# Optimization experiments

Hardware: AMD Instinct MI355X
Metric: run time of the kernel (lower is better)

The kernel has to match this reference:

```python
import jax, jax.numpy as jnp
import numpy as np

D = 512
H = 4 * D
EPS = 1e-5

def layernorm(x, g, b):
    mu = jnp.mean(x, axis=-1, keepdims=True)
    var = jnp.mean((x - mu) ** 2, axis=-1, keepdims=True)
    return (x - mu) * jax.lax.rsqrt(var + EPS) * g + b

def setup_inputs() -> dict:
    key = jax.random.key(0)
    ks = jax.random.split(key, 16)
    s = 0.02
    inp = {
        "x": jax.random.normal(ks[0], (16, 2048, D), dtype=jnp.float32),
        "wq": jax.random.normal(ks[1], (D, D), dtype=jnp.float32) * s,
        "bq": jnp.zeros((D,), jnp.float32),
        "wk": jax.random.normal(ks[2], (D, D), dtype=jnp.float32) * s,
        "bk": jnp.zeros((D,), jnp.float32),
        "wv": jax.random.normal(ks[3], (D, D), dtype=jnp.float32) * s,
        "bv": jnp.zeros((D,), jnp.float32),
        "wp": jax.random.normal(ks[4], (D, D), dtype=jnp.float32) * s,
        "bp": jnp.zeros((D,), jnp.float32),
        "w1": jax.random.normal(ks[5], (D, H), dtype=jnp.float32) * s,
        "b1": jnp.zeros((H,), jnp.float32),
        "w2": jax.random.normal(ks[6], (H, D), dtype=jnp.float32) * s,
        "b2": jnp.zeros((D,), jnp.float32),
        "g1": jnp.ones((D,), jnp.float32),
        "be1": jnp.zeros((D,), jnp.float32),
        "g2": jnp.ones((D,), jnp.float32),
        "be2": jnp.zeros((D,), jnp.float32),
    }
    return inp

def reference(x, wq, bq, wk, bk, wv, bv, wp, bp, w1, b1, w2, b2, g1, be1, g2, be2):
    temperature = jnp.sqrt(jnp.asarray(D, x.dtype))
    q = x @ wq + bq                      # [B,N,D]
    k = x @ wk + bk
    v = x @ wv + bv
    energy = jnp.einsum('bnd,bmd->bnm', q / temperature, k)   # [B,N,N]
    attn = jax.nn.softmax(energy, axis=-1)
    out = jnp.einsum('bnm,bmd->bnd', attn, v)
    att = out @ wp + bp
    x = layernorm(x + att, g1, be1)
    h = jax.nn.gelu(x @ w1 + b1, approximate=False)
    ff = h @ w2 + b2
    x = layernorm(x + ff, g2, be2)
    return x
```

## Files before the change

### kernel.cpp

```cpp
#include <hip/hip_runtime.h>
#include <cmath>

typedef __bf16 bf16_t;
typedef __bf16 bf16x8 __attribute__((ext_vector_type(8)));
typedef __bf16 bf16x4 __attribute__((ext_vector_type(4)));
typedef float f32x4 __attribute__((ext_vector_type(4)));

#define DEV_INLINE __device__ __forceinline__

DEV_INLINE void gload_lds16(const void* g, void* l) {
  __builtin_amdgcn_global_load_lds(
      (const __attribute__((address_space(1))) void*)g,
      (__attribute__((address_space(3))) void*)l, 16, 0, 0);
}

DEV_INLINE float gelu_f(float v) {
  const float u = v * (0.7978845608f + 0.0356774081f * v * v);
  const float e = __expf(2.f * u);
  const float th = 1.f - 2.f / (e + 1.f);
  return 0.5f * v * (1.f + th);
}

template<int EPI, bool HAS_BIAS>
__global__ __launch_bounds__(256, 2)
void gemm_bt(const bf16_t* __restrict__ A, const bf16_t* __restrict__ B,
             const float* __restrict__ bias, void* __restrict__ C,
             bf16_t* __restrict__ vTaux,
             int M, int N, int K, int lda, int ldb, int ldc,
             long sA, long sB, long sC, float scale)
{
  constexpr bool SWAP = (EPI == 1 || EPI == 2 || EPI == 3);
  __shared__ alignas(16) bf16_t lds[3][2][4096];
  const int b = blockIdx.z;
  A += (long)b * sA;
  B += (long)b * sB;
  const int t  = threadIdx.x;
  const int l  = t & 63;
  const int w  = t >> 6;
  const int wr = (w >> 1) * 64;
  const int wc = (w & 1) * 64;

  const int gx  = gridDim.x;
  const int nwg = gx * gridDim.y;
  int id = blockIdx.y * gx + blockIdx.x;
  id = (id & 7) * (nwg >> 3) + (id >> 3);
  const int m0 = (id / gx) * 128;
  const int n0 = (id % gx) * 128;

  const int r0 = t >> 2;
  const int r1 = r0 + 64;
  const int wb = (t & 3) * 16;
  const int cbs0 = wb ^ (((r0 >> 1) & 3) << 4);
  const int cbs1 = wb ^ (((r1 >> 1) & 3) << 4);
  const bf16_t* gA0 = A + (long)(m0 + r0) * lda + (cbs0 >> 1);
  const bf16_t* gA1 = A + (long)(m0 + r1) * lda + (cbs1 >> 1);
  const bf16_t* gB0 = B + (long)(n0 + r0) * ldb + (cbs0 >> 1);
  const bf16_t* gB1 = B + (long)(n0 + r1) * ldb + (cbs1 >> 1);

#define STAGE(kt, q) do {                                   \
    const long kofs_ = (long)(kt) * 32;                     \
    gload_lds16(gA0 + kofs_, &lds[q][0][t * 8]);            \
    gload_lds16(gA1 + kofs_, &lds[q][0][2048 + t * 8]);     \
    gload_lds16(gB0 + kofs_, &lds[q][1][t * 8]);            \
    gload_lds16(gB1 + kofs_, &lds[q][1][2048 + t * 8]);     \
  } while (0)

  const int fr  = l & 15;
  const int kkb = (l >> 4) * 16;
  int offA[4], offB[4];
#pragma unroll
  for (int mi = 0; mi < 4; mi++) {
    const int row = wr + mi * 16 + fr;
    offA[mi] = row * 32 + ((kkb ^ (((row >> 1) & 3) << 4)) >> 1);
  }
#pragma unroll
  for (int ni = 0; ni < 4; ni++) {
    const int row = wc + ni * 16 + fr;
    offB[ni] = row * 32 + ((kkb ^ (((row >> 1) & 3) << 4)) >> 1);
  }

  f32x4 acc[4][4] = {};

  const int NT = K >> 5;
  STAGE(0, 0);
  STAGE(1, 1);

  int q = 0;
  for (int kt = 0; kt < NT; ++kt) {
    if (kt < NT - 1) asm volatile("s_waitcnt vmcnt(4)" ::: "memory");
    else             asm volatile("s_waitcnt vmcnt(0)" ::: "memory");
    __builtin_amdgcn_sched_barrier(0);
    __builtin_amdgcn_s_barrier();

    if (kt + 2 < NT) {
      int qs = q + 2; if (qs >= 3) qs -= 3;
      STAGE(kt + 2, qs);
    }

    bf16x8 af[4], bfr[4];
#pragma unroll
    for (int mi = 0; mi < 4; mi++)
      af[mi] = *(const bf16x8*)&lds[q][0][offA[mi]];
#pragma unroll
    for (int ni = 0; ni < 4; ni++)
      bfr[ni] = *(const bf16x8*)&lds[q][1][offB[ni]];
#pragma unroll
    for (int mi = 0; mi < 4; mi++)
#pragma unroll
      for (int ni = 0; ni < 4; ni++) {
        if constexpr (SWAP)
          acc[mi][ni] = __builtin_amdgcn_mfma_f32_16x16x32_bf16(
              bfr[ni], af[mi], acc[mi][ni], 0, 0, 0);
        else
          acc[mi][ni] = __builtin_amdgcn_mfma_f32_16x16x32_bf16(
              af[mi], bfr[ni], acc[mi][ni], 0, 0, 0);
      }

    if (++q == 3) q = 0;
  }
#undef STAGE

  const long cb = (long)b * sC;

  if constexpr (SWAP) {
    const int cq = (l >> 4) * 4;
#pragma unroll
    for (int mi = 0; mi < 4; mi++) {
      const int row = m0 + wr + mi * 16 + fr;
      bf16_t* crow = (bf16_t*)C + cb + (long)row * ldc;
#pragma unroll
      for (int ni = 0; ni < 4; ni++) {
        const int c0 = n0 + wc + ni * 16 + cq;
        float4 b4 = {0.f, 0.f, 0.f, 0.f};
        if constexpr (HAS_BIAS) b4 = *(const float4*)&bias[c0];
        float vv[4] = { acc[mi][ni][0] + b4.x, acc[mi][ni][1] + b4.y,
                        acc[mi][ni][2] + b4.z, acc[mi][ni][3] + b4.w };
        if constexpr (EPI == 2) {
#pragma unroll
          for (int r = 0; r < 4; r++) vv[r] *= scale;
        }
        if constexpr (EPI == 3) {
#pragma unroll
          for (int r = 0; r < 4; r++) vv[r] = gelu_f(vv[r]);
        }
        bf16x4 pk = { (bf16_t)vv[0], (bf16_t)vv[1],
                      (bf16_t)vv[2], (bf16_t)vv[3] };
        *(bf16x4*)(crow + c0) = pk;
      }
    }
    return;
  }

  const int rbase = m0 + wr + (l >> 4) * 4;
#pragma unroll
  for (int mi = 0; mi < 4; mi++) {
    const int row0 = rbase + mi * 16;
#pragma unroll
    for (int ni = 0; ni < 4; ni++) {
      const int c = n0 + wc + ni * 16 + fr;
      float bias_v = 0.f;
      if constexpr (HAS_BIAS) bias_v = bias[c];
      float vals[4];
#pragma unroll
      for (int r = 0; r < 4; r++) vals[r] = acc[mi][ni][r] + bias_v;
      if (c < 1024) {
#pragma unroll
        for (int r = 0; r < 4; r++)
          ((bf16_t*)C)[(long)(row0 + r) * ldc + c] = (bf16_t)vals[r];
      } else {
        const int bb = row0 >> 11;
        const int n  = row0 & 2047;
        bf16x4 pk = { (bf16_t)vals[0], (bf16_t)vals[1],
                      (bf16_t)vals[2], (bf16_t)vals[3] };
        *(bf16x4*)&vTaux[(long)bb * (512 * 2048) + (long)(c - 1024) * 2048 + n] = pk;
      }
    }
  }
}

__global__ __launch_bounds__(256)
void transpose_cast(const float* __restrict__ in, bf16_t* __restrict__ out,
                    int R, int Cc)
{
  __shared__ float tile[32][33];
  const int c0 = blockIdx.x * 32;
  const int r0 = blockIdx.y * 32;
  const int tx = threadIdx.x & 31;
  const int ty = threadIdx.x >> 5;
#pragma unroll
  for (int i = 0; i < 32; i += 8)
    tile[ty + i][tx] = in[(long)(r0 + ty + i) * Cc + (c0 + tx)];
  __syncthreads();
#pragma unroll
  for (int i = 0; i < 32; i += 8)
    out[(long)(c0 + ty + i) * R + (r0 + tx)] = (bf16_t)tile[tx][ty + i];
}

__global__ __launch_bounds__(256)
void cast_to_bf16(const float* __restrict__ in, bf16_t* __restrict__ out, long n)
{
  const long i = ((long)blockIdx.x * 256 + threadIdx.x) * 4;
  if (i >= n) return;
  const float4 v = *(const float4*)&in[i];
  bf16x4 o = { (bf16_t)v.x, (bf16_t)v.y, (bf16_t)v.z, (bf16_t)v.w };
  *(bf16x4*)&out[i] = o;
}

__global__ __launch_bounds__(256)
void concat_bias(const float* __restrict__ a, const float* __restrict__ b,
                 const float* __restrict__ c, float* __restrict__ o)
{
  const int i = blockIdx.x * 256 + threadIdx.x;
  if (i < 512) o[i] = a[i];
  else if (i < 1024) o[i] = b[i - 512];
  else if (i < 1536) o[i] = c[i - 1024];
}

__global__ __launch_bounds__(256)
void softmax2048(bf16_t* __restrict__ E)
{
  const long row = blockIdx.x;
  bf16_t* p = E + row * 2048;
  const int t = threadIdx.x;
  bf16x8 xv = *(const bf16x8*)&p[t * 8];
  float v[8];
#pragma unroll
  for (int j = 0; j < 8; j++) v[j] = (float)xv[j];
  float m = v[0];
#pragma unroll
  for (int j = 1; j < 8; j++) m = fmaxf(m, v[j]);
  for (int o = 32; o; o >>= 1) m = fmaxf(m, __shfl_xor(m, o));
  __shared__ float redm[4];
  __shared__ float reds[4];
  if ((t & 63) == 0) redm[t >> 6] = m;
  __syncthreads();
  m = fmaxf(fmaxf(redm[0], redm[1]), fmaxf(redm[2], redm[3]));
  float s = 0.f;
#pragma unroll
  for (int j = 0; j < 8; j++) { v[j] = __expf(v[j] - m); s += v[j]; }
  for (int o = 32; o; o >>= 1) s += __shfl_xor(s, o);
  if ((t & 63) == 0) reds[t >> 6] = s;
  __syncthreads();
  s = reds[0] + reds[1] + reds[2] + reds[3];
  const float inv = 1.f / s;
  bf16x8 ov;
#pragma unroll
  for (int j = 0; j < 8; j++) ov[j] = (bf16_t)(v[j] * inv);
  *(bf16x8*)&p[t * 8] = ov;
}

template<bool EMIT_F32, bool EMIT_BF16>
__global__ __launch_bounds__(128)
void add_ln(const bf16_t* __restrict__ xa, const bf16_t* __restrict__ xadd,
            const float* __restrict__ g, const float* __restrict__ be,
            float* __restrict__ y, bf16_t* __restrict__ yb)
{
  const long row = blockIdx.x;
  const int c = threadIdx.x * 4;
  bf16x4 a = *(const bf16x4*)&xa[row * 512 + c];
  bf16x4 d = *(const bf16x4*)&xadd[row * 512 + c];
  float vv[4];
#pragma unroll
  for (int j = 0; j < 4; j++) vv[j] = (float)a[j] + (float)d[j];
  float s = 0.f, s2 = 0.f;
#pragma unroll
  for (int j = 0; j < 4; j++) { s += vv[j]; s2 += vv[j] * vv[j]; }
  for (int o = 32; o; o >>= 1) { s += __shfl_xor(s, o); s2 += __shfl_xor(s2, o); }
  __shared__ float r0[2], r1[2];
  const int w = threadIdx.x >> 6;
  if ((threadIdx.x & 63) == 0) { r0[w] = s; r1[w] = s2; }
  __syncthreads();
  s = r0[0] + r0[1]; s2 = r1[0] + r1[1];
  const float mu = s * (1.f / 512.f);
  const float var = s2 * (1.f / 512.f) - mu * mu;
  const float rstd = rsqrtf(var + 1e-5f);
  const float4 gg = *(const float4*)&g[c];
  const float4 bev = *(const float4*)&be[c];
  float o0 = (vv[0] - mu) * rstd * gg.x + bev.x;
  float o1 = (vv[1] - mu) * rstd * gg.y + bev.y;
  float o2 = (vv[2] - mu) * rstd * gg.z + bev.z;
  float o3 = (vv[3] - mu) * rstd * gg.w + bev.w;
  if constexpr (EMIT_F32) {
    float4 yo = { o0, o1, o2, o3 };
    *(float4*)&y[row * 512 + c] = yo;
  }
  if constexpr (EMIT_BF16) {
    bf16x4 ob = { (bf16_t)o0, (bf16_t)o1, (bf16_t)o2, (bf16_t)o3 };
    *(bf16x4*)&yb[row * 512 + c] = ob;
  }
}

extern "C" void kernel_launch(void* const* d_in, const int* in_sizes, int n_in,
                              void* d_out, int out_size, void* d_ws, size_t ws_size,
                              hipStream_t stream)
{
  const float* x   = (const float*)d_in[0];
  const float* wq  = (const float*)d_in[1];
  const float* bq  = (const float*)d_in[2];
  const float* wk  = (const float*)d_in[3];
  const float* bk  = (const float*)d_in[4];
  const float* wv  = (const float*)d_in[5];
  const float* bv  = (const float*)d_in[6];
  const float* wp  = (const float*)d_in[7];
  const float* bp  = (const float*)d_in[8];
  const float* w1  = (const float*)d_in[9];
  const float* b1  = (const float*)d_in[10];
  const float* w2  = (const float*)d_in[11];
  const float* b2  = (const float*)d_in[12];
  const float* g1  = (const float*)d_in[13];
  const float* be1 = (const float*)d_in[14];
  const float* g2  = (const float*)d_in[15];
  const float* be2 = (const float*)d_in[16];

  const long S = 16L * 2048 * 512;
  const long Mi = 1L << 20;

  const size_t NEED = (size_t)232 * Mi;
  if (ws_size < NEED) return;

  char* wsp = (char*)d_ws;
  bf16_t* wqkvT = (bf16_t*)(wsp + 0);
  bf16_t* wpT   = wqkvT + 1536L * 512;
  bf16_t* w1T   = wpT + 512L * 512;
  bf16_t* w2T   = w1T + 2048L * 512;
  float*  bqkv  = (float*)(w2T + 512L * 2048);
  bf16_t* xb    = (bf16_t*)(wsp +   8 * Mi);
  bf16_t* qkb   = (bf16_t*)(wsp +  40 * Mi);
  bf16_t* vT    = (bf16_t*)(wsp + 104 * Mi);
  bf16_t* E     = (bf16_t*)(wsp + 136 * Mi);
  bf16_t* ob    = (bf16_t*)(wsp + 200 * Mi);
  bf16_t* x1b   = qkb;
  bf16_t* h     = (bf16_t*)(wsp + 72 * Mi);
  bf16_t* projb = E;
  bf16_t* ffb   = xb;

  cast_to_bf16<<<dim3((unsigned)(S / 4 / 256)), 256, 0, stream>>>(x, xb, S);

  transpose_cast<<<dim3(16, 16), 256, 0, stream>>>(wq, wqkvT,               512, 512);
  transpose_cast<<<dim3(16, 16), 256, 0, stream>>>(wk, wqkvT + 512L * 512,  512, 512);
  transpose_cast<<<dim3(16, 16), 256, 0, stream>>>(wv, wqkvT + 1024L * 512, 512, 512);
  transpose_cast<<<dim3(16, 16), 256, 0, stream>>>(wp, wpT, 512, 512);
  transpose_cast<<<dim3(64, 16), 256, 0, stream>>>(w1, w1T, 512, 2048);
  transpose_cast<<<dim3(16, 64), 256, 0, stream>>>(w2, w2T, 2048, 512);
  concat_bias<<<dim3(6), 256, 0, stream>>>(bq, bk, bv, bqkv);

  gemm_bt<5, true><<<dim3(12, 256, 1), 256, 0, stream>>>(
      xb, wqkvT, bqkv, qkb, vT, 32768, 1536, 512, 512, 512, 1024, 0, 0, 0, 0.f);

  for (int cgrp = 0; cgrp < 2; cgrp++) {
    const long qoff = (long)cgrp * 8 * 2048 * 1024;
    gemm_bt<2, false><<<dim3(16, 16, 8), 256, 0, stream>>>(
        qkb + qoff, qkb + qoff + 512, nullptr, E, nullptr,
        2048, 2048, 512, 1024, 1024, 2048,
        2048L * 1024, 2048L * 1024, 2048L * 2048, 0.04419417382f);
    softmax2048<<<dim3(16384), 256, 0, stream>>>(E);
    gemm_bt<1, false><<<dim3(4, 16, 8), 256, 0, stream>>>(
        E, vT + (long)cgrp * 8 * 512 * 2048, nullptr,
        ob + (long)cgrp * 8 * 2048 * 512, nullptr,
        2048, 512, 2048, 2048, 2048, 512,
        2048L * 2048, 512L * 2048, 2048L * 512, 0.f);
  }

  gemm_bt<1, true><<<dim3(4, 256, 1), 256, 0, stream>>>(
      ob, wpT, bp, projb, nullptr,
      32768, 512, 512, 512, 512, 512, 0, 0, 0, 0.f);

  add_ln<false, true><<<dim3(32768), 128, 0, stream>>>(
      xb, projb, g1, be1, nullptr, x1b);

  gemm_bt<3, true><<<dim3(16, 256, 1), 256, 0, stream>>>(
      x1b, w1T, b1, h, nullptr, 32768, 2048, 512, 512, 512, 2048, 0, 0, 0, 0.f);

  gemm_bt<1, true><<<dim3(4, 256, 1), 256, 0, stream>>>(
      h, w2T, b2, ffb, nullptr,
      32768, 512, 2048, 2048, 2048, 512, 0, 0, 0, 0.f);

  add_ln<true, false><<<dim3(32768), 128, 0, stream>>>(
      x1b, ffb, g2, be2, (float*)d_out, nullptr);
}
```

Measured before the change: 615.7 us.

## Add 128x256-tile GEMM kernel for QK^T and FFN1 GEMMs

Adds a new GEMM kernel with a 128x256 output tile, where each of the four waves computes a 64x128 sub-tile, using a 3-stage LDS pipeline and XOR-swizzled loads. The QK^T energy GEMM and the FFN up-projection with GELU now use it in place of the generic 128x128 kernel. The larger N tile raises arithmetic intensity and reuse of the A operand, which cuts global and LDS traffic per FLOP. In exchange it needs more accumulator registers (128 floats per thread) and more LDS, which may lower occupancy or cause spills under launch_bounds(256,2).

Result: no change. 620.0 us (+0.7%).

```diff
diff --git a/kernel.cpp b/kernel.cpp
--- a/kernel.cpp
+++ b/kernel.cpp
@@ -19,6 +19,130 @@
   const float e = __expf(2.f * u);
   const float th = 1.f - 2.f / (e + 1.f);
   return 0.5f * v * (1.f + th);
+}
+
+template<int EPI, bool HAS_BIAS>
+__global__ __launch_bounds__(256, 2)
+void gemm_n256(const bf16_t* __restrict__ A, const bf16_t* __restrict__ B,
+               const float* __restrict__ bias, bf16_t* __restrict__ C,
+               int M, int N, int K, int lda, int ldb, int ldc,
+               long sA, long sB, long sC, float scale)
+{
+  __shared__ alignas(16) bf16_t As[3][4096];
+  __shared__ alignas(16) bf16_t Bs[3][8192];
+  const int b = blockIdx.z;
+  A += (long)b * sA;
+  B += (long)b * sB;
+  const int t  = threadIdx.x;
+  const int l  = t & 63;
+  const int w  = t >> 6;
+  const int wr   = (w >> 1) * 64;
+  const int wcol = (w & 1) * 128;
+
+  const int gx  = gridDim.x;
+  const int nwg = gx * gridDim.y;
+  int id = blockIdx.y * gx + blockIdx.x;
+  id = (id & 7) * (nwg >> 3) + (id >> 3);
+  const int m0 = (id / gx) * 128;
+  const int n0 = (id % gx) * 256;
+
+  const int r0 = t >> 2;
+  const int wb = (t & 3) * 16;
+  const int cbs = wb ^ (((r0 >> 1) & 3) << 4);
+  const bf16_t* gA0 = A + (long)(m0 + r0) * lda + (cbs >> 1);
+  const bf16_t* gA1 = A + (long)(m0 + r0 + 64) * lda + (cbs >> 1);
+  const bf16_t* gB0 = B + (long)(n0 + r0) * ldb + (cbs >> 1);
+
+#define STAGE6(kt, q) do {                                       \
+    const long ko_ = (long)(kt) * 32;                            \
+    gload_lds16(gA0 + ko_, &As[q][t * 8]);                       \
+    gload_lds16(gA1 + ko_, &As[q][2048 + t * 8]);                \
+    gload_lds16(gB0 + ko_,                   &Bs[q][t * 8]);     \
+    gload_lds16(gB0 +  64 * (long)ldb + ko_, &Bs[q][2048 + t * 8]); \
+    gload_lds16(gB0 + 128 * (long)ldb + ko_, &Bs[q][4096 + t * 8]); \
+    gload_lds16(gB0 + 192 * (long)ldb + ko_, &Bs[q][6144 + t * 8]); \
+  } while (0)
+
+  const int fr  = l & 15;
+  const int kkb = (l >> 4) * 16;
+  int offA[4], offB[8];
+#pragma unroll
+  for (int mi = 0; mi < 4; mi++) {
+    const int row = wr + mi * 16 + fr;
+    offA[mi] = row * 32 + ((kkb ^ (((row >> 1) & 3) << 4)) >> 1);
+  }
+#pragma unroll
+  for (int ni = 0; ni < 8; ni++) {
+    const int row = wcol + ni * 16 + fr;
+    offB[ni] = row * 32 + ((kkb ^ (((row >> 1) & 3) << 4)) >> 1);
+  }
+
+  f32x4 acc[4][8] = {};
+
+  const int NT = K >> 5;
+  STAGE6(0, 0);
+  STAGE6(1, 1);
+
+  int q = 0;
+  for (int kt = 0; kt < NT; ++kt) {
+    if (kt < NT - 1) asm volatile("s_waitcnt vmcnt(6)" ::: "memory");
+    else             asm volatile("s_waitcnt vmcnt(0)" ::: "memory");
+    __builtin_amdgcn_sched_barrier(0);
+    __builtin_amdgcn_s_barrier();
+
+    if (kt + 2 < NT) {
+      int qs = q + 2; if (qs >= 3) qs -= 3;
+      STAGE6(kt + 2, qs);
+    }
+
+    bf16x8 af[4];
+#pragma unroll
+    for (int mi = 0; mi < 4; mi++)
+      af[mi] = *(const bf16x8*)&As[q][offA[mi]];
+#pragma unroll
+    for (int nh = 0; nh < 2; nh++) {
+      bf16x8 bf4[4];
+#pragma unroll
+      for (int nj = 0; nj < 4; nj++)
+        bf4[nj] = *(const bf16x8*)&Bs[q][offB[nh * 4 + nj]];
+#pragma unroll
+      for (int mi = 0; mi < 4; mi++)
+#pragma unroll
+        for (int nj = 0; nj < 4; nj++)
+          acc[mi][nh * 4 + nj] = __builtin_amdgcn_mfma_f32_16x16x32_bf16(
+              bf4[nj], af[mi], acc[mi][nh * 4 + nj], 0, 0, 0);
+    }
+
+    if (++q == 3) q = 0;
+  }
+#undef STAGE6
+
+  const long cb = (long)b * sC;
+  const int cq = (l >> 4) * 4;
+#pragma unroll
+  for (int mi = 0; mi < 4; mi++) {
+    const int row = m0 + wr + mi * 16 + fr;
+    bf16_t* crow = C + cb + (long)row * ldc;
+#pragma unroll
+    for (int ni = 0; ni < 8; ni++) {
+      const int c0 = n0 + wcol + ni * 16 + cq;
+      float4 b4 = {0.f, 0.f, 0.f, 0.f};
+      if constexpr (HAS_BIAS) b4 = *(const float4*)&bias[c0];
+      float vv[4] = { acc[mi][ni][0] + b4.x, acc[mi][ni][1] + b4.y,
+                      acc[mi][ni][2] + b4.z, acc[mi][ni][3] + b4.w };
+      if constexpr (EPI == 2) {
+#pragma unroll
+        for (int r = 0; r < 4; r++) vv[r] *= scale;
+      }
+      if constexpr (EPI == 3) {
+#pragma unroll
+        for (int r = 0; r < 4; r++) vv[r] = gelu_f(vv[r]);
+      }
+      bf16x4 pk = { (bf16_t)vv[0], (bf16_t)vv[1],
+                    (bf16_t)vv[2], (bf16_t)vv[3] };
+      *(bf16x4*)(crow + c0) = pk;
+    }
+  }
 }
 
 template<int EPI, bool HAS_BIAS>
@@ -349,8 +473,8 @@
 
   for (int cgrp = 0; cgrp < 2; cgrp++) {
     const long qoff = (long)cgrp * 8 * 2048 * 1024;
-    gemm_bt<2, false><<<dim3(16, 16, 8), 256, 0, stream>>>(
-        qkb + qoff, qkb + qoff + 512, nullptr, E, nullptr,
+    gemm_n256<2, false><<<dim3(8, 16, 8), 256, 0, stream>>>(
+        qkb + qoff, qkb + qoff + 512, nullptr, E,
         2048, 2048, 512, 1024, 1024, 2048,
         2048L * 1024, 2048L * 1024, 2048L * 2048, 0.04419417382f);
     softmax2048<<<dim3(16384), 256, 0, stream>>>(E);
@@ -368,8 +492,8 @@
   add_ln<false, true><<<dim3(32768), 128, 0, stream>>>(
       xb, projb, g1, be1, nullptr, x1b);
 
-  gemm_bt<3, true><<<dim3(16, 256, 1), 256, 0, stream>>>(
-      x1b, w1T, b1, h, nullptr, 32768, 2048, 512, 512, 512, 2048, 0, 0, 0, 0.f);
+  gemm_n256<3, true><<<dim3(8, 256, 1), 256, 0, stream>>>(
+      x1b, w1T, b1, h, 32768, 2048, 512, 512, 512, 2048, 0, 0, 0, 0.f);
 
   gemm_bt<1, true><<<dim3(4, 256, 1), 256, 0, stream>>>(
       h, w2T, b2, ffb, nullptr,
```
